# Optimization experiments

Measured on AMD Instinct MI355X. Metric: run time of the kernel, lower is better.

Reference implementation:

```python
import jax, jax.numpy as jnp
import numpy as np

B, S, D, H = 1, 4096, 768, 12
Dh = D // H  # 64


def setup_inputs() -> dict:
    key = jax.random.key(0)
    ks = jax.random.split(key, 11)
    w = lambda k, sh: jax.random.normal(k, sh, jnp.float32) * 0.02
    return {
        "query": jax.random.normal(ks[0], (B, S, D), jnp.float32),
        "key": jax.random.normal(ks[1], (B, S, D), jnp.float32),
        "value": jax.random.normal(ks[2], (B, S, D), jnp.float32),
        "mask": jnp.ones((B, S), jnp.int32),  # nonzero = attend; mask==0 positions are filled with -inf
        "Wq": w(ks[3], (D, D)), "bq": w(ks[4], (D,)),
        "Wk": w(ks[5], (D, D)), "bk": w(ks[6], (D,)),
        "Wv": w(ks[7], (D, D)), "bv": w(ks[8], (D,)),
        "Wo": w(ks[9], (D, D)), "bo": w(ks[10], (D,)),
    }


def reference(query, key, value, mask, Wq, bq, Wk, bk, Wv, bv, Wo, bo):
    # shape(): (B, S, D) -> (B, H, S, Dh)
    def split_heads(x):
        return x.reshape(B, S, H, Dh).transpose(0, 2, 1, 3)

    q = split_heads(query @ Wq.T + bq) / np.sqrt(Dh).astype(np.float32)
    k = split_heads(key @ Wk.T + bk)
    # multi_rand_attn_cuda is an unbiased randomized estimator of
    # weights @ v_lin(value); the exact-math baseline applies v_lin then
    # contracts with the attention weights per head.
    v = split_heads(value @ Wv.T + bv)

    scores = jnp.einsum('bhqd,bhkd->bhqk', q, k)  # (B,H,S,S)
    scores = jnp.where((mask == 0)[:, None, None, :], -jnp.inf, scores)
    weights = jax.nn.softmax(scores, axis=-1)  # dropout is identity at eval

    ctx = jnp.einsum('bhqk,bhkd->bhqd', weights, v)
    ctx = ctx.transpose(0, 2, 1, 3).reshape(B, S, D)  # unshape
    return ctx @ Wo.T + bo
```

## Files before the change

kernel.cpp:

```cpp
#include <hip/hip_runtime.h>

#define S_LEN 4096
#define D_MODEL 768
#define N_HEADS 12
#define D_HEAD 64

typedef short bf16x8 __attribute__((ext_vector_type(8)));
typedef float f32x4 __attribute__((ext_vector_type(4)));
typedef float f32x16 __attribute__((ext_vector_type(16)));
typedef float f32x4v __attribute__((ext_vector_type(4)));
typedef unsigned short u16;
typedef unsigned short u16x8 __attribute__((ext_vector_type(8)));
typedef unsigned int u32;

__device__ __forceinline__ u16 f2bf(float f) {
  unsigned u = __float_as_uint(f);
  u += 0x7FFFu + ((u >> 16) & 1u);
  return (u16)(u >> 16);
}

__device__ __forceinline__ u32 pk2bf(float lo, float hi) {
  u32 a = __float_as_uint(hi) + 0x8000u;
  u32 b = __float_as_uint(lo) + 0x8000u;
  return __builtin_amdgcn_perm(a, b, 0x07060302u);
}

__device__ __forceinline__ void gl_lds16(const void* g, void* l) {
  __builtin_amdgcn_global_load_lds(
      (const __attribute__((address_space(1))) void*)g,
      (__attribute__((address_space(3))) void*)l, 16, 0, 0);
}

struct CvtArgs {
  const float* s[4];
  u16* d[4];
};

__global__ __launch_bounds__(256) void cvt8_kernel(CvtArgs a, long n) {
  const float* s = a.s[blockIdx.z];
  u16* d = a.d[blockIdx.z];
  long i = ((long)blockIdx.x * 256 + threadIdx.x) * 8;
  if (i >= n) return;
  f32x4v v0 = *(const f32x4v*)(s + i);
  f32x4v v1 = *(const f32x4v*)(s + i + 4);
  u16x8 o;
#pragma unroll
  for (int j = 0; j < 4; ++j) { o[j] = f2bf(v0[j]); o[j + 4] = f2bf(v1[j]); }
  *(u16x8*)(d + i) = o;
}

struct ProjArgs {
  const u16* A[3];
  const u16* W[3];
  const float* bias[3];
  void* out[3];
  float scale[3];
  int mode[3];
};

__global__ __launch_bounds__(256, 2) void proj_kernel(ProjArgs args) {
  const int z = blockIdx.z;
  const u16* __restrict__ A = args.A[z];
  const u16* __restrict__ W = args.W[z];
  const float* __restrict__ bias = args.bias[z];
  const float scale = args.scale[z];
  const int mode = args.mode[z];

  __shared__ u16 Al[128 * 32];
  __shared__ u16 Bl[128 * 32];

  const int tid = threadIdx.x;
  const int w = tid >> 6, l = tid & 63;
  const int l15 = l & 15, quad = l >> 4;
  const int m0 = blockIdx.x * 128;
  const int n0 = blockIdx.y * 128;
  const int wm = (w & 1) * 64, wn = (w >> 1) * 64;
  const int crow = l >> 2, ccol = (l & 3) * 8;

  f32x4 acc[4][4] = {};

  for (int kt = 0; kt < 24; ++kt) {
    const int k0 = kt * 32;
#pragma unroll
    for (int i = 0; i < 2; ++i) {
      const int sub = w * 2 + i;
      const int row = sub * 16 + crow;
      gl_lds16(&A[(size_t)(m0 + row) * D_MODEL + k0 + ccol], &Al[sub * 512 + l * 8]);
      gl_lds16(&W[(size_t)(n0 + row) * D_MODEL + k0 + ccol], &Bl[sub * 512 + l * 8]);
    }
    __syncthreads();
    bf16x8 af[4], bfr[4];
#pragma unroll
    for (int mf = 0; mf < 4; ++mf)
      af[mf] = *(const bf16x8*)&Al[(wm + mf * 16 + l15) * 32 + quad * 8];
#pragma unroll
    for (int nf = 0; nf < 4; ++nf)
      bfr[nf] = *(const bf16x8*)&Bl[(wn + nf * 16 + l15) * 32 + quad * 8];
#pragma unroll
    for (int mf = 0; mf < 4; ++mf)
#pragma unroll
      for (int nf = 0; nf < 4; ++nf)
        acc[mf][nf] = __builtin_amdgcn_mfma_f32_16x16x32_bf16(af[mf], bfr[nf], acc[mf][nf], 0, 0, 0);
    __syncthreads();
  }

#pragma unroll
  for (int nf = 0; nf < 4; ++nf) {
    const int col = n0 + wn + nf * 16 + l15;
    const float bv = bias[col];
#pragma unroll
    for (int mf = 0; mf < 4; ++mf) {
#pragma unroll
      for (int r = 0; r < 4; ++r) {
        const int row = m0 + wm + mf * 16 + quad * 4 + r;
        const float v = (acc[mf][nf][r] + bv) * scale;
        if (mode == 0) {
          ((u16*)args.out[z])[(size_t)row * D_MODEL + col] = f2bf(v);
        } else if (mode == 2) {
          ((float*)args.out[z])[(size_t)row * D_MODEL + col] = v;
        } else if (mode == 3) {
          const int hh = col >> 6, d = col & 63;
          const int st = row >> 5, kl = row & 31;
          const int s = d >> 4, gg = (d >> 3) & 1, j = d & 7;
          ((u16*)args.out[z])[(size_t)((hh * 128 + st) * 4 + s) * 512 + (gg * 32 + kl) * 8 + j] = f2bf(v);
        } else {
          const int hh = col >> 6, d = col & 63;
          const int st = row >> 5, r16 = row & 15, u = (row >> 4) & 1;
          const int j = (r16 & 3) | (((r16 >> 3) & 1) << 2);
          const int gg = (r16 >> 2) & 1;
          const int db = (d >> 5) & 1, vl = d & 31;
          ((u16*)args.out[z])[(size_t)((hh * 128 + st) * 4 + db * 2 + u) * 512 + (gg * 32 + vl) * 8 + j] = f2bf(v);
        }
      }
    }
  }
}

__global__ __launch_bounds__(256, 2) void flash_kernel(
    const u16* __restrict__ Qb, const u16* __restrict__ Kpk,
    const u16* __restrict__ Vpk, const int* __restrict__ mask,
    u16* __restrict__ Ctx) {
  __shared__ char smem[67584];

  const int tid = threadIdx.x;
  const int w = tid >> 6, l = tid & 63;
  const int l31 = l & 31, g = l >> 5;
  const int h = blockIdx.y;
  const int q0 = blockIdx.x * 64;

  bf16x8 qf[2][4];
#pragma unroll
  for (int qs = 0; qs < 2; ++qs) {
    const u16* qrow = Qb + (size_t)(q0 + qs * 32 + l31) * D_MODEL + h * D_HEAD + g * 8;
#pragma unroll
    for (int s = 0; s < 4; ++s) qf[qs][s] = *(const bf16x8*)(qrow + s * 16);
  }

  const char* kg = (const char*)(Kpk + ((size_t)h * 128 + w) * 2048);
  const char* vg = (const char*)(Vpk + ((size_t)h * 128 + w) * 2048);
  char* stg = smem + w * 16384;
  const size_t lo = (size_t)l * 16;

  f32x16 oacc[2][2] = {};
  float lsum[2] = {0.f, 0.f};
  int mv[2];

  mv[0] = mask[w * 32 + l31];
#pragma unroll
  for (int c = 0; c < 4; ++c) gl_lds16(kg + c * 1024 + lo, stg + c * 1024);
#pragma unroll
  for (int c = 0; c < 4; ++c) gl_lds16(vg + c * 1024 + lo, stg + 4096 + c * 1024);

  int buf = 0;
  for (int it = 0; it < 32; ++it) {
    char* cb = stg + buf * 8192;
    __builtin_amdgcn_s_waitcnt(0x0F70);
    const unsigned long long mb = __ballot(mv[buf] != 0);
    bf16x8 kf[4], vf[4];
#pragma unroll
    for (int c = 0; c < 4; ++c) kf[c] = *(const bf16x8*)(cb + c * 1024 + lo);
#pragma unroll
    for (int c = 0; c < 4; ++c) vf[c] = *(const bf16x8*)(cb + 4096 + c * 1024 + lo);

    if (it < 31) {
      char* nb = stg + (buf ^ 1) * 8192;
      const char* kn = kg + (size_t)(it + 1) * 16384;
      const char* vn = vg + (size_t)(it + 1) * 16384;
      mv[buf ^ 1] = mask[(w + 4 * (it + 1)) * 32 + l31];
#pragma unroll
      for (int c = 0; c < 4; ++c) gl_lds16(kn + c * 1024 + lo, nb + c * 1024);
#pragma unroll
      for (int c = 0; c < 4; ++c) gl_lds16(vn + c * 1024 + lo, nb + 4096 + c * 1024);
    }

#pragma unroll
    for (int qs = 0; qs < 2; ++qs) {
      f32x16 sacc = {};
#pragma unroll
      for (int s = 0; s < 4; ++s)
        sacc = __builtin_amdgcn_mfma_f32_32x32x16_bf16(kf[s], qf[qs][s], sacc, 0, 0, 0);

#pragma unroll
      for (int r = 0; r < 16; ++r) sacc[r] = __builtin_amdgcn_exp2f(sacc[r]);
      if (mb + 1ull != 0ull) {
        const unsigned mh = (unsigned)(mb >> (4 * g));
#pragma unroll
        for (int r = 0; r < 16; ++r)
          if (!((mh >> ((r & 3) + 8 * (r >> 2))) & 1u)) sacc[r] = 0.f;
      }
      float ts = 0.f;
#pragma unroll
      for (int r = 0; r < 16; ++r) ts += sacc[r];
      lsum[qs] += ts;

      u32 pk[8];
#pragma unroll
      for (int i = 0; i < 8; ++i) pk[i] = pk2bf(sacc[2 * i], sacc[2 * i + 1]);
#pragma unroll
      for (int u = 0; u < 2; ++u) {
        union { u32 u4[4]; bf16x8 s; } bp;
#pragma unroll
        for (int i = 0; i < 4; ++i) bp.u4[i] = pk[4 * u + i];
        oacc[qs][0] = __builtin_amdgcn_mfma_f32_32x32x16_bf16(vf[u], bp.s, oacc[qs][0], 0, 0, 0);
        oacc[qs][1] = __builtin_amdgcn_mfma_f32_32x32x16_bf16(vf[2 + u], bp.s, oacc[qs][1], 0, 0, 0);
      }
    }
    buf ^= 1;
  }

  __syncthreads();
  float* Ol = (float*)smem;
  float* Ll = (float*)(smem + 65536);
#pragma unroll
  for (int qs = 0; qs < 2; ++qs)
#pragma unroll
    for (int db = 0; db < 2; ++db)
#pragma unroll
      for (int r = 0; r < 16; ++r)
        Ol[((w * 4 + qs * 2 + db) * 16 + r) * 64 + l] = oacc[qs][db][r];
#pragma unroll
  for (int qs = 0; qs < 2; ++qs) Ll[w * 128 + qs * 64 + l] = lsum[qs];
  __syncthreads();

#pragma unroll
  for (int qs = 0; qs < 2; ++qs) {
    float Lt = 0.f;
#pragma unroll
    for (int w2 = 0; w2 < 4; ++w2)
      Lt += Ll[w2 * 128 + qs * 64 + l] + Ll[w2 * 128 + qs * 64 + (l ^ 32)];
    const float linv = 1.0f / Lt;
#pragma unroll
    for (int db = 0; db < 2; ++db) {
      float v[4];
#pragma unroll
      for (int i = 0; i < 4; ++i) {
        const int r = w * 4 + i;
        float acc = 0.f;
#pragma unroll
        for (int w2 = 0; w2 < 4; ++w2)
          acc += Ol[((w2 * 4 + qs * 2 + db) * 16 + r) * 64 + l];
        v[i] = acc * linv;
      }
      u16* cp = Ctx + (size_t)(q0 + qs * 32 + l31) * D_MODEL + h * D_HEAD + db * 32 + w * 8 + 4 * g;
      *(u32*)(cp) = pk2bf(v[0], v[1]);
      *(u32*)(cp + 2) = pk2bf(v[2], v[3]);
    }
  }
}

extern "C" void kernel_launch(void* const* d_in, const int* in_sizes, int n_in,
                              void* d_out, int out_size, void* d_ws, size_t ws_size,
                              hipStream_t stream) {
  const float* query = (const float*)d_in[0];
  const float* key   = (const float*)d_in[1];
  const float* value = (const float*)d_in[2];
  const int*   maskp = (const int*)d_in[3];
  const float* Wq = (const float*)d_in[4];
  const float* bq = (const float*)d_in[5];
  const float* Wk = (const float*)d_in[6];
  const float* bk = (const float*)d_in[7];
  const float* Wv = (const float*)d_in[8];
  const float* bv = (const float*)d_in[9];
  const float* Wo = (const float*)d_in[10];
  const float* bo = (const float*)d_in[11];

  char* ws = (char*)d_ws;
  const size_t SZX = (size_t)S_LEN * D_MODEL * 2;
  const size_t SZW = (size_t)D_MODEL * D_MODEL * 2;
  u16* Xq  = (u16*)(ws);
  u16* Xk  = (u16*)(ws + SZX);
  u16* Xv  = (u16*)(ws + 2 * SZX);
  u16* Qb  = (u16*)(ws + 3 * SZX);
  u16* Kpk = (u16*)(ws + 4 * SZX);
  u16* Vpk = (u16*)(ws + 5 * SZX);
  u16* Wqb = (u16*)(ws + 6 * SZX);
  u16* Wkb = (u16*)(ws + 6 * SZX + SZW);
  u16* Wvb = (u16*)(ws + 6 * SZX + 2 * SZW);
  u16* Wob = (u16*)(ws + 6 * SZX + 3 * SZW);
  u16* Ctx = Xq;

  CvtArgs ca;
  ca.s[0] = query; ca.s[1] = key; ca.s[2] = value; ca.s[3] = query;
  ca.d[0] = Xq;    ca.d[1] = Xk;  ca.d[2] = Xv;    ca.d[3] = Xq;
  cvt8_kernel<<<dim3(1536, 1, 3), 256, 0, stream>>>(ca, (long)S_LEN * D_MODEL);

  CvtArgs cw;
  cw.s[0] = Wq;  cw.s[1] = Wk;  cw.s[2] = Wv;  cw.s[3] = Wo;
  cw.d[0] = Wqb; cw.d[1] = Wkb; cw.d[2] = Wvb; cw.d[3] = Wob;
  cvt8_kernel<<<dim3(288, 1, 4), 256, 0, stream>>>(cw, (long)D_MODEL * D_MODEL);

  ProjArgs pa;
  pa.A[0] = Xq;  pa.A[1] = Xk;  pa.A[2] = Xv;
  pa.W[0] = Wqb; pa.W[1] = Wkb; pa.W[2] = Wvb;
  pa.bias[0] = bq; pa.bias[1] = bk; pa.bias[2] = bv;
  pa.out[0] = Qb; pa.out[1] = Kpk; pa.out[2] = Vpk;
  pa.scale[0] = 0.125f * 1.4426950408889634f; pa.scale[1] = 1.f; pa.scale[2] = 1.f;
  pa.mode[0] = 0; pa.mode[1] = 3; pa.mode[2] = 4;
  proj_kernel<<<dim3(32, 6, 3), 256, 0, stream>>>(pa);

  flash_kernel<<<dim3(64, N_HEADS, 1), 256, 0, stream>>>(Qb, Kpk, Vpk, maskp, Ctx);

  ProjArgs po;
  po.A[0] = Ctx; po.A[1] = Ctx; po.A[2] = Ctx;
  po.W[0] = Wob; po.W[1] = Wob; po.W[2] = Wob;
  po.bias[0] = bo; po.bias[1] = bo; po.bias[2] = bo;
  po.out[0] = d_out; po.out[1] = d_out; po.out[2] = d_out;
  po.scale[0] = 1.f; po.scale[1] = 1.f; po.scale[2] = 1.f;
  po.mode[0] = 2; po.mode[1] = 2; po.mode[2] = 2;
  proj_kernel<<<dim3(32, 6, 1), 256, 0, stream>>>(po);
}
```

Baseline: 225.4 us.

## Split flash-attention work across wave pairs and shrink output-projection tiles

The flash kernel now gives each pair of waves one 32-row query slice and half of the key range. One wave of the pair streams K and the other streams V into a shared double buffer, synchronised with block barriers. This halves the per-wave register and LDS footprint, so occupancy can rise to three blocks per CU, but it adds a __syncthreads on every iteration. Separately, the projection kernel is templated on the M tile, and the output projection uses 64-row tiles to launch twice as many blocks and fill the GPU better.

Measured after the change: 218.0 us. 1.03x faster.

```diff
diff --git a/kernel.cpp b/kernel.cpp
--- a/kernel.cpp
+++ b/kernel.cpp
@@ -58,7 +58,10 @@
   int mode[3];
 };
 
-__global__ __launch_bounds__(256, 2) void proj_kernel(ProjArgs args) {
+template <int TM>
+__global__ __launch_bounds__(256, TM == 128 ? 2 : 4) void proj_kernel(ProjArgs args) {
+  constexpr int MF = TM / 32;
+  constexpr int CA = TM / 16;
   const int z = blockIdx.z;
   const u16* __restrict__ A = args.A[z];
   const u16* __restrict__ W = args.W[z];
@@ -66,38 +69,43 @@
   const float scale = args.scale[z];
   const int mode = args.mode[z];
 
-  __shared__ u16 Al[128 * 32];
+  __shared__ u16 Al[TM * 32];
   __shared__ u16 Bl[128 * 32];
 
   const int tid = threadIdx.x;
   const int w = tid >> 6, l = tid & 63;
   const int l15 = l & 15, quad = l >> 4;
-  const int m0 = blockIdx.x * 128;
+  const int m0 = blockIdx.x * TM;
   const int n0 = blockIdx.y * 128;
-  const int wm = (w & 1) * 64, wn = (w >> 1) * 64;
+  const int wm = (w & 1) * (TM / 2), wn = (w >> 1) * 64;
   const int crow = l >> 2, ccol = (l & 3) * 8;
 
-  f32x4 acc[4][4] = {};
+  f32x4 acc[MF][4] = {};
 
   for (int kt = 0; kt < 24; ++kt) {
     const int k0 = kt * 32;
+#pragma unroll
+    for (int i = 0; i < CA / 4; ++i) {
+      const int sub = w * (CA / 4) + i;
+      const int row = sub * 16 + crow;
+      gl_lds16(&A[(size_t)(m0 + row) * D_MODEL + k0 + ccol], &Al[sub * 512 + l * 8]);
+    }
 #pragma unroll
     for (int i = 0; i < 2; ++i) {
       const int sub = w * 2 + i;
       const int row = sub * 16 + crow;
-      gl_lds16(&A[(size_t)(m0 + row) * D_MODEL + k0 + ccol], &Al[sub * 512 + l * 8]);
       gl_lds16(&W[(size_t)(n0 + row) * D_MODEL + k0 + ccol], &Bl[sub * 512 + l * 8]);
     }
     __syncthreads();
-    bf16x8 af[4], bfr[4];
-#pragma unroll
-    for (int mf = 0; mf < 4; ++mf)
+    bf16x8 af[MF], bfr[4];
+#pragma unroll
+    for (int mf = 0; mf < MF; ++mf)
       af[mf] = *(const bf16x8*)&Al[(wm + mf * 16 + l15) * 32 + quad * 8];
 #pragma unroll
     for (int nf = 0; nf < 4; ++nf)
       bfr[nf] = *(const bf16x8*)&Bl[(wn + nf * 16 + l15) * 32 + quad * 8];
 #pragma unroll
-    for (int mf = 0; mf < 4; ++mf)
+    for (int mf = 0; mf < MF; ++mf)
 #pragma unroll
       for (int nf = 0; nf < 4; ++nf)
         acc[mf][nf] = __builtin_amdgcn_mfma_f32_16x16x32_bf16(af[mf], bfr[nf], acc[mf][nf], 0, 0, 0);
@@ -109,7 +117,7 @@
     const int col = n0 + wn + nf * 16 + l15;
     const float bv = bias[col];
 #pragma unroll
-    for (int mf = 0; mf < 4; ++mf) {
+    for (int mf = 0; mf < MF; ++mf) {
 #pragma unroll
       for (int r = 0; r < 4; ++r) {
         const int row = m0 + wm + mf * 16 + quad * 4 + r;
@@ -136,135 +144,117 @@
   }
 }
 
-__global__ __launch_bounds__(256, 2) void flash_kernel(
+__global__ __launch_bounds__(256, 3) void flash_kernel(
     const u16* __restrict__ Qb, const u16* __restrict__ Kpk,
     const u16* __restrict__ Vpk, const int* __restrict__ mask,
     u16* __restrict__ Ctx) {
-  __shared__ char smem[67584];
+  __shared__ char smem[33792];
 
   const int tid = threadIdx.x;
   const int w = tid >> 6, l = tid & 63;
   const int l31 = l & 31, g = l >> 5;
+  const int a = w & 1, b = w >> 1;
   const int h = blockIdx.y;
-  const int q0 = blockIdx.x * 64;
-
-  bf16x8 qf[2][4];
-#pragma unroll
-  for (int qs = 0; qs < 2; ++qs) {
-    const u16* qrow = Qb + (size_t)(q0 + qs * 32 + l31) * D_MODEL + h * D_HEAD + g * 8;
-#pragma unroll
-    for (int s = 0; s < 4; ++s) qf[qs][s] = *(const bf16x8*)(qrow + s * 16);
-  }
-
-  const char* kg = (const char*)(Kpk + ((size_t)h * 128 + w) * 2048);
-  const char* vg = (const char*)(Vpk + ((size_t)h * 128 + w) * 2048);
-  char* stg = smem + w * 16384;
+  const int q0 = blockIdx.x * 64 + a * 32;
+
+  bf16x8 qf[4];
+  {
+    const u16* qrow = Qb + (size_t)(q0 + l31) * D_MODEL + h * D_HEAD + g * 8;
+#pragma unroll
+    for (int s = 0; s < 4; ++s) qf[s] = *(const bf16x8*)(qrow + s * 16);
+  }
+
+  const char* kvg = a ? (const char*)(Vpk + ((size_t)h * 128 + b * 64) * 2048)
+                      : (const char*)(Kpk + ((size_t)h * 128 + b * 64) * 2048);
+  char* pair = smem + b * 16384;
+  const int akv = a * 4096;
   const size_t lo = (size_t)l * 16;
 
-  f32x16 oacc[2][2] = {};
-  float lsum[2] = {0.f, 0.f};
+  f32x16 oacc0 = {}, oacc1 = {};
+  float lsum = 0.f;
   int mv[2];
 
-  mv[0] = mask[w * 32 + l31];
-#pragma unroll
-  for (int c = 0; c < 4; ++c) gl_lds16(kg + c * 1024 + lo, stg + c * 1024);
-#pragma unroll
-  for (int c = 0; c < 4; ++c) gl_lds16(vg + c * 1024 + lo, stg + 4096 + c * 1024);
+  mv[0] = mask[b * 2048 + l31];
+#pragma unroll
+  for (int c = 0; c < 4; ++c) gl_lds16(kvg + c * 1024 + lo, pair + akv + c * 1024);
 
   int buf = 0;
-  for (int it = 0; it < 32; ++it) {
-    char* cb = stg + buf * 8192;
-    __builtin_amdgcn_s_waitcnt(0x0F70);
+  for (int it = 0; it < 64; ++it) {
+    __syncthreads();
     const unsigned long long mb = __ballot(mv[buf] != 0);
+    const char* cb = pair + buf * 8192;
     bf16x8 kf[4], vf[4];
 #pragma unroll
     for (int c = 0; c < 4; ++c) kf[c] = *(const bf16x8*)(cb + c * 1024 + lo);
 #pragma unroll
     for (int c = 0; c < 4; ++c) vf[c] = *(const bf16x8*)(cb + 4096 + c * 1024 + lo);
 
-    if (it < 31) {
-      char* nb = stg + (buf ^ 1) * 8192;
-      const char* kn = kg + (size_t)(it + 1) * 16384;
-      const char* vn = vg + (size_t)(it + 1) * 16384;
-      mv[buf ^ 1] = mask[(w + 4 * (it + 1)) * 32 + l31];
-#pragma unroll
-      for (int c = 0; c < 4; ++c) gl_lds16(kn + c * 1024 + lo, nb + c * 1024);
-#pragma unroll
-      for (int c = 0; c < 4; ++c) gl_lds16(vn + c * 1024 + lo, nb + 4096 + c * 1024);
-    }
-
-#pragma unroll
-    for (int qs = 0; qs < 2; ++qs) {
-      f32x16 sacc = {};
-#pragma unroll
-      for (int s = 0; s < 4; ++s)
-        sacc = __builtin_amdgcn_mfma_f32_32x32x16_bf16(kf[s], qf[qs][s], sacc, 0, 0, 0);
-
-#pragma unroll
-      for (int r = 0; r < 16; ++r) sacc[r] = __builtin_amdgcn_exp2f(sacc[r]);
-      if (mb + 1ull != 0ull) {
-        const unsigned mh = (unsigned)(mb >> (4 * g));
-#pragma unroll
-        for (int r = 0; r < 16; ++r)
-          if (!((mh >> ((r & 3) + 8 * (r >> 2))) & 1u)) sacc[r] = 0.f;
-      }
-      float ts = 0.f;
-#pragma unroll
-      for (int r = 0; r < 16; ++r) ts += sacc[r];
-      lsum[qs] += ts;
-
-      u32 pk[8];
-#pragma unroll
-      for (int i = 0; i < 8; ++i) pk[i] = pk2bf(sacc[2 * i], sacc[2 * i + 1]);
-#pragma unroll
-      for (int u = 0; u < 2; ++u) {
-        union { u32 u4[4]; bf16x8 s; } bp;
-#pragma unroll
-        for (int i = 0; i < 4; ++i) bp.u4[i] = pk[4 * u + i];
-        oacc[qs][0] = __builtin_amdgcn_mfma_f32_32x32x16_bf16(vf[u], bp.s, oacc[qs][0], 0, 0, 0);
-        oacc[qs][1] = __builtin_amdgcn_mfma_f32_32x32x16_bf16(vf[2 + u], bp.s, oacc[qs][1], 0, 0, 0);
-      }
+    if (it < 63) {
+      mv[buf ^ 1] = mask[(b * 64 + it + 1) * 32 + l31];
+      char* nb = pair + (buf ^ 1) * 8192 + akv;
+      const char* src = kvg + (size_t)(it + 1) * 4096;
+#pragma unroll
+      for (int c = 0; c < 4; ++c) gl_lds16(src + c * 1024 + lo, nb + c * 1024);
+    }
+
+    f32x16 sacc = {};
+#pragma unroll
+    for (int s = 0; s < 4; ++s)
+      sacc = __builtin_amdgcn_mfma_f32_32x32x16_bf16(kf[s], qf[s], sacc, 0, 0, 0);
+
+#pragma unroll
+    for (int r = 0; r < 16; ++r) sacc[r] = __builtin_amdgcn_exp2f(sacc[r]);
+    if (mb + 1ull != 0ull) {
+      const unsigned mh = (unsigned)(mb >> (4 * g));
+#pragma unroll
+      for (int r = 0; r < 16; ++r)
+        if (!((mh >> ((r & 3) + 8 * (r >> 2))) & 1u)) sacc[r] = 0.f;
+    }
+    float ts = 0.f;
+#pragma unroll
+    for (int r = 0; r < 16; ++r) ts += sacc[r];
+    lsum += ts;
+
+    u32 pk[8];
+#pragma unroll
+    for (int i = 0; i < 8; ++i) pk[i] = pk2bf(sacc[2 * i], sacc[2 * i + 1]);
+#pragma unroll
+    for (int u = 0; u < 2; ++u) {
+      union { u32 u4[4]; bf16x8 s; } bp;
+#pragma unroll
+      for (int i = 0; i < 4; ++i) bp.u4[i] = pk[4 * u + i];
+      oacc0 = __builtin_amdgcn_mfma_f32_32x32x16_bf16(vf[u], bp.s, oacc0, 0, 0, 0);
+      oacc1 = __builtin_amdgcn_mfma_f32_32x32x16_bf16(vf[2 + u], bp.s, oacc1, 0, 0, 0);
     }
     buf ^= 1;
   }
 
   __syncthreads();
   float* Ol = (float*)smem;
-  float* Ll = (float*)(smem + 65536);
-#pragma unroll
-  for (int qs = 0; qs < 2; ++qs)
-#pragma unroll
-    for (int db = 0; db < 2; ++db)
-#pragma unroll
-      for (int r = 0; r < 16; ++r)
-        Ol[((w * 4 + qs * 2 + db) * 16 + r) * 64 + l] = oacc[qs][db][r];
-#pragma unroll
-  for (int qs = 0; qs < 2; ++qs) Ll[w * 128 + qs * 64 + l] = lsum[qs];
+  float* Ll = (float*)(smem + 32768);
+#pragma unroll
+  for (int r = 0; r < 16; ++r) {
+    Ol[((w * 2 + 0) * 16 + r) * 64 + l] = oacc0[r];
+    Ol[((w * 2 + 1) * 16 + r) * 64 + l] = oacc1[r];
+  }
+  Ll[w * 64 + l] = lsum;
   __syncthreads();
 
-#pragma unroll
-  for (int qs = 0; qs < 2; ++qs) {
-    float Lt = 0.f;
-#pragma unroll
-    for (int w2 = 0; w2 < 4; ++w2)
-      Lt += Ll[w2 * 128 + qs * 64 + l] + Ll[w2 * 128 + qs * 64 + (l ^ 32)];
-    const float linv = 1.0f / Lt;
-#pragma unroll
-    for (int db = 0; db < 2; ++db) {
-      float v[4];
-#pragma unroll
-      for (int i = 0; i < 4; ++i) {
-        const int r = w * 4 + i;
-        float acc = 0.f;
-#pragma unroll
-        for (int w2 = 0; w2 < 4; ++w2)
-          acc += Ol[((w2 * 4 + qs * 2 + db) * 16 + r) * 64 + l];
-        v[i] = acc * linv;
-      }
-      u16* cp = Ctx + (size_t)(q0 + qs * 32 + l31) * D_MODEL + h * D_HEAD + db * 32 + w * 8 + 4 * g;
-      *(u32*)(cp) = pk2bf(v[0], v[1]);
-      *(u32*)(cp + 2) = pk2bf(v[2], v[3]);
-    }
+  float Lt = Ll[a * 64 + l] + Ll[a * 64 + (l ^ 32)] +
+             Ll[(a + 2) * 64 + l] + Ll[(a + 2) * 64 + (l ^ 32)];
+  const float linv = 1.0f / Lt;
+#pragma unroll
+  for (int rr = 0; rr < 4; ++rr) {
+    float v[4];
+#pragma unroll
+    for (int i = 0; i < 4; ++i) {
+      const int r = rr * 4 + i;
+      v[i] = (Ol[((a * 2 + b) * 16 + r) * 64 + l] +
+              Ol[((a * 2 + 4 + b) * 16 + r) * 64 + l]) * linv;
+    }
+    u16* cp = Ctx + (size_t)(q0 + l31) * D_MODEL + h * D_HEAD + b * 32 + rr * 8 + 4 * g;
+    *(u32*)(cp) = pk2bf(v[0], v[1]);
+    *(u32*)(cp + 2) = pk2bf(v[2], v[3]);
   }
 }
 
@@ -316,7 +306,7 @@
   pa.out[0] = Qb; pa.out[1] = Kpk; pa.out[2] = Vpk;
   pa.scale[0] = 0.125f * 1.4426950408889634f; pa.scale[1] = 1.f; pa.scale[2] = 1.f;
   pa.mode[0] = 0; pa.mode[1] = 3; pa.mode[2] = 4;
-  proj_kernel<<<dim3(32, 6, 3), 256, 0, stream>>>(pa);
+  proj_kernel<128><<<dim3(32, 6, 3), 256, 0, stream>>>(pa);
 
   flash_kernel<<<dim3(64, N_HEADS, 1), 256, 0, stream>>>(Qb, Kpk, Vpk, maskp, Ctx);
 
@@ -327,5 +317,5 @@
   po.out[0] = d_out; po.out[1] = d_out; po.out[2] = d_out;
   po.scale[0] = 1.f; po.scale[1] = 1.f; po.scale[2] = 1.f;
   po.mode[0] = 2; po.mode[1] = 2; po.mode[2] = 2;
-  proj_kernel<<<dim3(32, 6, 1), 256, 0, stream>>>(po);
-}
+  proj_kernel<64><<<dim3(64, 6, 1), 256, 0, stream>>>(po);
+}
```
